# Optimization experiments

Measured on AMD Instinct MI355X. Metric: run time of the kernel, lower is better.

## Reference

```python
import jax, jax.numpy as jnp
import numpy as np

EMBED = 64
MAX_LEN = 256
EPS = 1e-5

def layernorm(x, g, b):
    mu = jnp.mean(x, axis=-1, keepdims=True)
    var = jnp.mean(jnp.square(x - mu), axis=-1, keepdims=True)
    return (x - mu) * jax.lax.rsqrt(var + EPS) * g + b

def setup_inputs() -> dict:
    key = jax.random.key(0)
    ks = jax.random.split(key, 10)
    V = 50257
    B, T = 32, 256
    s = 1.0 / np.sqrt(EMBED)
    return {
        "x": jax.random.randint(ks[0], (B, T), 0, V),
        "embed_w": jax.random.normal(ks[1], (V, EMBED), jnp.float32) * 0.02,
        "pos_w": jax.random.normal(ks[2], (MAX_LEN, EMBED), jnp.float32) * 0.02,
        "ln1_g": jnp.ones((EMBED,), jnp.float32),
        "ln1_b": jnp.zeros((EMBED,), jnp.float32),
        "Wq": jax.random.normal(ks[3], (EMBED, EMBED), jnp.float32) * s,
        "Wk": jax.random.normal(ks[4], (EMBED, EMBED), jnp.float32) * s,
        "Wv": jax.random.normal(ks[5], (EMBED, EMBED), jnp.float32) * s,
        "lnf_g": jnp.ones((EMBED,), jnp.float32),
        "lnf_b": jnp.zeros((EMBED,), jnp.float32),
        "fc_w": jax.random.normal(ks[6], (EMBED, V), jnp.float32) * s,
        "fc_b": jnp.zeros((V,), jnp.float32),
    }

def reference(x, embed_w, pos_w, ln1_g, ln1_b, Wq, Wk, Wv, lnf_g, lnf_b, fc_w, fc_b):
    B, T = x.shape
    tok = embed_w[x]                       # [B,T,E]
    pos = pos_w[:T][None, :, :]            # [1,T,E]
    h = tok + pos
    hn = layernorm(h, ln1_g, ln1_b)
    Q = hn @ Wq
    K = hn @ Wk
    V = hn @ Wv
    att = jnp.einsum('bqe,bke->bqk', Q, K) / jnp.sqrt(jnp.float32(EMBED))
    causal = jnp.tril(jnp.ones((T, T), bool))
    att = jnp.where(causal, att, -jnp.inf)
    att = jax.nn.softmax(att, axis=-1)
    ctx = jnp.einsum('bqk,bke->bqe', att, V)  # dropout = identity (eval mode)
    h = h + ctx
    h = layernorm(h, lnf_g, lnf_b)
    logits = h @ fc_w + fc_b               # [B,T,vocab]
    return logits
```

## Files before the change

### kernel.cpp

```cpp
#include <hip/hip_runtime.h>
#include <hip/hip_bf16.h>

#define EMBED  64
#define TLEN   256
#define BATCH  32
#define NROWS  (BATCH*TLEN)
#define VOCAB  50257
#define BCOLS  256
#define NB     198
#define VPAD   (NB*BCOLS)
#define LNEPS  1e-5f

typedef __attribute__((ext_vector_type(8))) short  bf16x8;
typedef __attribute__((ext_vector_type(4))) float  f32x4;
typedef __attribute__((ext_vector_type(4))) unsigned int u32x4;

static __device__ __forceinline__ unsigned short f2bf(float f) {
    unsigned int u = __float_as_uint(f);
    unsigned int r = (u + 0x7fffu + ((u >> 16) & 1u)) >> 16;
    return (unsigned short)r;
}

__global__ __launch_bounds__(256) void prep_wt(const float* __restrict__ fcw,
                                               unsigned short* __restrict__ wt) {
    int n = blockIdx.x * 256 + threadIdx.x;
    if (n >= VPAD) return;
    unsigned int packed[32];
    if (n < VOCAB) {
        #pragma unroll
        for (int k2 = 0; k2 < 32; ++k2) {
            unsigned int lo = f2bf(fcw[(size_t)(2*k2)   * VOCAB + n]);
            unsigned int hi = f2bf(fcw[(size_t)(2*k2+1) * VOCAB + n]);
            packed[k2] = lo | (hi << 16);
        }
    } else {
        #pragma unroll
        for (int k2 = 0; k2 < 32; ++k2) packed[k2] = 0u;
    }
    u32x4* dst = (u32x4*)(wt + (size_t)n * 64);
    #pragma unroll
    for (int i = 0; i < 8; ++i) {
        u32x4 v = { packed[4*i], packed[4*i+1], packed[4*i+2], packed[4*i+3] };
        dst[i] = v;
    }
}

__global__ __launch_bounds__(256) void embed_ln(const int* __restrict__ x,
                                                const float* __restrict__ ew,
                                                const float* __restrict__ pw,
                                                const float* __restrict__ g,
                                                const float* __restrict__ bb,
                                                float* __restrict__ h,
                                                float* __restrict__ hn) {
    int row = blockIdx.x * 4 + (threadIdx.x >> 6);
    int e   = threadIdx.x & 63;
    int tok = x[row];
    float v = ew[(size_t)tok * 64 + e] + pw[(size_t)(row & 255) * 64 + e];
    h[(size_t)row * 64 + e] = v;
    float s = v;
    #pragma unroll
    for (int m = 32; m >= 1; m >>= 1) s += __shfl_xor(s, m, 64);
    float mu = s * (1.f/64.f);
    float d  = v - mu;
    float s2 = d * d;
    #pragma unroll
    for (int m = 32; m >= 1; m >>= 1) s2 += __shfl_xor(s2, m, 64);
    float var = s2 * (1.f/64.f);
    hn[(size_t)row * 64 + e] = d * rsqrtf(var + LNEPS) * g[e] + bb[e];
}

__global__ __launch_bounds__(192) void qkv(const float* __restrict__ hn,
                                           const float* __restrict__ wq,
                                           const float* __restrict__ wk,
                                           const float* __restrict__ wv,
                                           float* __restrict__ q,
                                           float* __restrict__ kt,
                                           float* __restrict__ v) {
    int wave = threadIdx.x >> 6;
    int j    = threadIdx.x & 63;
    const float* W = (wave == 0) ? wq : ((wave == 1) ? wk : wv);
    int m0 = blockIdx.x * 16;
    for (int r = 0; r < 16; ++r) {
        int m = m0 + r;
        const float* hr = hn + (size_t)m * 64;
        float acc = 0.f;
        #pragma unroll
        for (int e = 0; e < 64; ++e) acc += hr[e] * W[e * 64 + j];
        if (wave == 0)      q[(size_t)m * 64 + j] = acc;
        else if (wave == 1) {
            int b = m >> 8, t = m & 255;
            kt[((size_t)b * 64 + j) * 256 + t] = acc;
        } else              v[(size_t)m * 64 + j] = acc;
    }
}

__global__ __launch_bounds__(256) void attn_sm(const float* __restrict__ q,
                                               const float* __restrict__ kt,
                                               float* __restrict__ p) {
    int b   = blockIdx.y;
    int m4  = blockIdx.x;
    int key = threadIdx.x;
    int wave = key >> 6, lane = key & 63;
    const float* ktb = kt + (size_t)b * 64 * 256;
    const float* qb  = q  + ((size_t)b * 256 + m4 * 4) * 64;
    float s0=0.f, s1=0.f, s2=0.f, s3=0.f;
    for (int e = 0; e < 64; ++e) {
        float kv = ktb[e * 256 + key];
        s0 += qb[e]       * kv;
        s1 += qb[64 + e]  * kv;
        s2 += qb[128 + e] * kv;
        s3 += qb[192 + e] * kv;
    }
    float sv[4] = { s0*0.125f, s1*0.125f, s2*0.125f, s3*0.125f };
    __shared__ float redm[4][4], reds[4][4];
    float pe[4];
    #pragma unroll
    for (int r = 0; r < 4; ++r) {
        int mrow = m4 * 4 + r;
        float xv = (key <= mrow) ? sv[r] : -1e30f;
        sv[r] = xv;
        float wm = xv;
        #pragma unroll
        for (int mm = 32; mm >= 1; mm >>= 1) wm = fmaxf(wm, __shfl_xor(wm, mm, 64));
        if (lane == 0) redm[wave][r] = wm;
    }
    __syncthreads();
    #pragma unroll
    for (int r = 0; r < 4; ++r) {
        float M = fmaxf(fmaxf(redm[0][r], redm[1][r]), fmaxf(redm[2][r], redm[3][r]));
        float e_ = expf(sv[r] - M);
        pe[r] = e_;
        float ws = e_;
        #pragma unroll
        for (int mm = 32; mm >= 1; mm >>= 1) ws += __shfl_xor(ws, mm, 64);
        if (lane == 0) reds[wave][r] = ws;
    }
    __syncthreads();
    float* pb = p + ((size_t)b * 256 + m4 * 4) * 256;
    #pragma unroll
    for (int r = 0; r < 4; ++r) {
        float S = reds[0][r] + reds[1][r] + reds[2][r] + reds[3][r];
        pb[r * 256 + key] = pe[r] / S;
    }
}

__global__ __launch_bounds__(256) void ctx_lnf(const float* __restrict__ p,
                                               const float* __restrict__ v,
                                               const float* __restrict__ h,
                                               const float* __restrict__ g,
                                               const float* __restrict__ bb,
                                               unsigned short* __restrict__ hf) {
    int m = blockIdx.x * 4 + (threadIdx.x >> 6);
    int n = threadIdx.x & 63;
    int b = m >> 8, t = m & 255;
    const float* pr = p + ((size_t)b * 256 + t) * 256;
    const float* vb = v + (size_t)b * 256 * 64;
    float acc = 0.f;
    for (int key = 0; key <= t; ++key)
        acc += pr[key] * vb[key * 64 + n];
    float h2 = h[(size_t)m * 64 + n] + acc;
    float s = h2;
    #pragma unroll
    for (int mm = 32; mm >= 1; mm >>= 1) s += __shfl_xor(s, mm, 64);
    float mu = s * (1.f/64.f);
    float d  = h2 - mu;
    float s2 = d * d;
    #pragma unroll
    for (int mm = 32; mm >= 1; mm >>= 1) s2 += __shfl_xor(s2, mm, 64);
    float var = s2 * (1.f/64.f);
    hf[(size_t)m * 64 + n] = f2bf(d * rsqrtf(var + LNEPS) * g[n] + bb[n]);
}

__global__ __launch_bounds__(256) void final_gemm(const unsigned short* __restrict__ hf,
                                                  const unsigned short* __restrict__ wt,
                                                  const float* __restrict__ bias,
                                                  float* __restrict__ out) {
    int bid = blockIdx.x;
    int xcd = bid & 7;
    int j   = bid >> 3;
    int g   = j / 1584;
    int rj  = j - g * 1584;
    int nb  = rj >> 3;
    int mb  = xcd * 64 + g * 8 + (rj & 7);
    int m0  = mb * 16;
    int cb  = nb * BCOLS;

    int tid  = threadIdx.x;
    int wave = tid >> 6, lane = tid & 63;
    int l15 = lane & 15, lk = lane >> 4;

    __shared__ float lds[16][260];

    const bf16x8* hrow = (const bf16x8*)(hf + (size_t)(m0 + l15) * 64);
    bf16x8 hb0 = hrow[lk];
    bf16x8 hb1 = hrow[4 + lk];

    #pragma unroll
    for (int nt = 0; nt < 4; ++nt) {
        int lcol = wave * 64 + nt * 16;
        const bf16x8* wrow = (const bf16x8*)(wt + (size_t)(cb + lcol + l15) * 64);
        f32x4 c = {0.f, 0.f, 0.f, 0.f};
        c = __builtin_amdgcn_mfma_f32_16x16x32_bf16(wrow[lk],     hb0, c, 0, 0, 0);
        c = __builtin_amdgcn_mfma_f32_16x16x32_bf16(wrow[4 + lk], hb1, c, 0, 0, 0);
        int bc = cb + lcol + lk * 4;
        if (bc + 4 <= VOCAB) {
            c += *(const f32x4*)(bias + bc);
        } else {
            #pragma unroll
            for (int e = 0; e < 4; ++e)
                c[e] += (bc + e < VOCAB) ? bias[bc + e] : 0.f;
        }
        *(f32x4*)&lds[l15][lcol + lk * 4] = c;
    }
    __syncthreads();

    int row = tid >> 4, cc = tid & 15;
    float* orow = out + (size_t)(m0 + row) * VOCAB + cb;
    const float* lrow = &lds[row][0];
    #pragma unroll
    for (int i = 0; i < 4; ++i) {
        int lcol = i * 64 + cc * 4;
        f32x4 vv = *(const f32x4*)(lrow + lcol);
        int cs = cb + lcol;
        if (cs + 4 <= VOCAB) {
            *(f32x4*)(orow + lcol) = vv;
        } else {
            #pragma unroll
            for (int e = 0; e < 4; ++e)
                if (cs + e < VOCAB) orow[lcol + e] = vv[e];
        }
    }
}

extern "C" void kernel_launch(void* const* d_in, const int* in_sizes, int n_in,
                              void* d_out, int out_size, void* d_ws, size_t ws_size,
                              hipStream_t stream) {
    const int*   x    = (const int*)  d_in[0];
    const float* ew   = (const float*)d_in[1];
    const float* pw   = (const float*)d_in[2];
    const float* ln1g = (const float*)d_in[3];
    const float* ln1b = (const float*)d_in[4];
    const float* wq   = (const float*)d_in[5];
    const float* wk   = (const float*)d_in[6];
    const float* wv   = (const float*)d_in[7];
    const float* lnfg = (const float*)d_in[8];
    const float* lnfb = (const float*)d_in[9];
    const float* fcw  = (const float*)d_in[10];
    const float* fcb  = (const float*)d_in[11];
    float* out = (float*)d_out;

    char* ws = (char*)d_ws;
    float*          h  = (float*)(ws + 0);
    float*          hn = (float*)(ws + (2u<<20));
    unsigned short* hf = (unsigned short*)(ws + (2u<<20));
    float*          q  = (float*)(ws + (4u<<20));
    float*          kt = (float*)(ws + (6u<<20));
    float*          v  = (float*)(ws + (8u<<20));
    float*          p  = (float*)(ws + (10u<<20));
    unsigned short* wt = (unsigned short*)(ws + (18u<<20));

    prep_wt  <<<dim3(VPAD / 256),  dim3(256), 0, stream>>>(fcw, wt);
    embed_ln <<<dim3(NROWS / 4),   dim3(256), 0, stream>>>(x, ew, pw, ln1g, ln1b, h, hn);
    qkv      <<<dim3(NROWS / 16),  dim3(192), 0, stream>>>(hn, wq, wk, wv, q, kt, v);
    attn_sm  <<<dim3(64, 32),      dim3(256), 0, stream>>>(q, kt, p);
    ctx_lnf  <<<dim3(NROWS / 4),   dim3(256), 0, stream>>>(p, v, h, lnfg, lnfb, hf);
    final_gemm<<<dim3(8 * 8 * NB * 8), dim3(256), 0, stream>>>(hf, wt, fcb, out);
}
```

Baseline: 695.4 us.

## Widen final GEMM column tile and store MFMA results directly to global

Doubles the per-block column tile of the vocabulary projection to 512 columns (halving the block count) and gives each wave 8 MFMA tiles instead of 4. The LDS staging buffer and __syncthreads are removed, so each lane writes its 4 accumulator floats straight to global memory. This drops the LDS round-trip and barrier, but the direct stores are now 16-byte pieces scattered over 16 rows instead of row-contiguous coalesced writes. VOCAB rows are not 16-byte aligned, so the vector stores may also be misaligned. The output write is the dominant cost, so the store pattern matters most.

After: 1.152 ms. 1.66x slower.

```diff
diff --git a/kernel.cpp b/kernel.cpp
--- a/kernel.cpp
+++ b/kernel.cpp
@@ -6,8 +6,8 @@
 #define BATCH  32
 #define NROWS  (BATCH*TLEN)
 #define VOCAB  50257
-#define BCOLS  256
-#define NB     198
+#define BCOLS  512
+#define NB     99
 #define VPAD   (NB*BCOLS)
 #define LNEPS  1e-5f
 
@@ -178,56 +178,37 @@
     int bid = blockIdx.x;
     int xcd = bid & 7;
     int j   = bid >> 3;
-    int g   = j / 1584;
-    int rj  = j - g * 1584;
+    int g   = j / 792;
+    int rj  = j - g * 792;
     int nb  = rj >> 3;
     int mb  = xcd * 64 + g * 8 + (rj & 7);
     int m0  = mb * 16;
     int cb  = nb * BCOLS;
 
-    int tid  = threadIdx.x;
-    int wave = tid >> 6, lane = tid & 63;
+    int wave = threadIdx.x >> 6, lane = threadIdx.x & 63;
     int l15 = lane & 15, lk = lane >> 4;
-
-    __shared__ float lds[16][260];
 
     const bf16x8* hrow = (const bf16x8*)(hf + (size_t)(m0 + l15) * 64);
     bf16x8 hb0 = hrow[lk];
     bf16x8 hb1 = hrow[4 + lk];
 
-    #pragma unroll
-    for (int nt = 0; nt < 4; ++nt) {
-        int lcol = wave * 64 + nt * 16;
+    float* orow = out + (size_t)(m0 + l15) * VOCAB;
+
+    #pragma unroll
+    for (int nt = 0; nt < 8; ++nt) {
+        int lcol = wave * 128 + nt * 16;
         const bf16x8* wrow = (const bf16x8*)(wt + (size_t)(cb + lcol + l15) * 64);
         f32x4 c = {0.f, 0.f, 0.f, 0.f};
         c = __builtin_amdgcn_mfma_f32_16x16x32_bf16(wrow[lk],     hb0, c, 0, 0, 0);
         c = __builtin_amdgcn_mfma_f32_16x16x32_bf16(wrow[4 + lk], hb1, c, 0, 0, 0);
-        int bc = cb + lcol + lk * 4;
-        if (bc + 4 <= VOCAB) {
-            c += *(const f32x4*)(bias + bc);
+        int vc = cb + lcol + lk * 4;
+        if (vc + 4 <= VOCAB) {
+            c += *(const f32x4*)(bias + vc);
+            *(f32x4*)(orow + vc) = c;
         } else {
             #pragma unroll
             for (int e = 0; e < 4; ++e)
-                c[e] += (bc + e < VOCAB) ? bias[bc + e] : 0.f;
-        }
-        *(f32x4*)&lds[l15][lcol + lk * 4] = c;
-    }
-    __syncthreads();
-
-    int row = tid >> 4, cc = tid & 15;
-    float* orow = out + (size_t)(m0 + row) * VOCAB + cb;
-    const float* lrow = &lds[row][0];
-    #pragma unroll
-    for (int i = 0; i < 4; ++i) {
-        int lcol = i * 64 + cc * 4;
-        f32x4 vv = *(const f32x4*)(lrow + lcol);
-        int cs = cb + lcol;
-        if (cs + 4 <= VOCAB) {
-            *(f32x4*)(orow + lcol) = vv;
-        } else {
-            #pragma unroll
-            for (int e = 0; e < 4; ++e)
-                if (cs + e < VOCAB) orow[lcol + e] = vv[e];
+                if (vc + e < VOCAB) orow[vc + e] = c[e] + bias[vc + e];
         }
     }
 }
```
